# Kernel optimization log

Measured on AMD Instinct MI355X. Metric: run time of the kernel, lower is better.

Reference implementation:

```python
import jax, jax.numpy as jnp
import numpy as np

B, S, D = 1024, 256, 256  # batch, n_class, feature dim (g = n_component = 1)


def setup_inputs() -> dict:
    key = jax.random.key(0)
    k1, k2, k3 = jax.random.split(key, 3)
    x = jax.random.normal(k1, (B, D), dtype=jnp.float32)
    mu_p = jax.random.normal(k2, (S, 1, D), dtype=jnp.float32)
    sigma_p = jax.random.normal(k3, (S, 1, D, D), dtype=jnp.float32)
    return {"x": x, "mu_p": mu_p, "sigma_p": sigma_p}


def _log_probs(x, mu_p, sigma_p):
    sp = sigma_p[:, 0]            # (S, D, D), component index g=0
    mu = mu_p[:, 0]               # (S, D)
    # parameter_enforcing: m = sigma_p^T @ sigma_p (PSD);
    # mean of (real) eigenvalues of m == trace(m)/D, so the ridge term is
    # 0.01 * (trace(m)/D) * I, making sigma symmetric positive definite.
    m = jnp.einsum('skd,ske->sde', sp, sp)                      # (S, D, D)
    ridge = 0.01 * (jnp.trace(m, axis1=-2, axis2=-1) / D)       # (S,)
    sigma = m + ridge[:, None, None] * jnp.eye(D, dtype=m.dtype)
    # MVN log_prob via Cholesky: logdet = 2*sum(log diag L),
    # maha = || L^{-1} (x - mu) ||^2
    L = jnp.linalg.cholesky(sigma)                              # (S, D, D)
    logdet = 2.0 * jnp.sum(jnp.log(jnp.diagonal(L, axis1=-2, axis2=-1)), -1)  # (S,)
    diff = x[None, :, :] - mu[:, None, :]                       # (S, B, D)
    # batched triangular solve per class: y = L^{-1} diff^T -> (S, D, B)
    y = jax.vmap(lambda Ls, ds: jax.scipy.linalg.solve_triangular(Ls, ds.T, lower=True))(L, diff)
    maha = jnp.sum(y * y, axis=1)                               # (S, B)
    log2pi = jnp.log(2.0 * jnp.pi).astype(x.dtype)
    logp = -0.5 * (D * log2pi + logdet[:, None] + maha)         # (S, B)
    return logp.T                                               # (B, S)


def reference(x, mu_p, sigma_p):
    return _log_probs(x, mu_p, sigma_p)
```

## Files before the change

### kernel.cpp

```cpp
#include <hip/hip_runtime.h>
#include <math.h>


#define LOG2PI_D 470.4965290007924f

typedef __attribute__((ext_vector_type(8))) short bf16x8;
typedef __attribute__((ext_vector_type(4))) float f32x4;

__device__ __forceinline__ unsigned bf16rtn(float f) {
  unsigned u = __float_as_uint(f);
  return (u + 0x7FFFu + ((u >> 16) & 1u)) >> 16;
}
__device__ __forceinline__ unsigned packhl(float v) {
  unsigned h = bf16rtn(v);
  float hf = __uint_as_float(h << 16);
  unsigned l = bf16rtn(v - hf);
  return (h << 16) | l;
}

__global__ __launch_bounds__(256) void k_gram(const float* __restrict__ sp,
                                              float* __restrict__ L,
                                              float* __restrict__ ridge_out) {
  __shared__ unsigned Hb[4 * 128 * 20];
  unsigned* AH = Hb;
  unsigned* AL = Hb + 128 * 20;
  unsigned* BH = Hb + 2 * 128 * 20;
  unsigned* BL = Hb + 3 * 128 * 20;
  int p = blockIdx.y, s = blockIdx.x;
  int bi = (p ? 128 : 0), bj = (p == 2 ? 128 : 0);
  const float* A = sp + (size_t)s * 65536;
  float* C = L + (size_t)s * 65536;
  int tid = threadIdx.x, w = tid >> 6, lane = tid & 63;
  int q = lane >> 4, n = lane & 15;
  int mt_[2] = {w, 7 - w};
  f32x4 acc[2][8] = {};
  int c = tid & 127, g = tid >> 7;

  float va[16], vb[16];
#pragma unroll
  for (int u = 0; u < 16; ++u) {
    va[u] = A[(size_t)(g * 16 + u) * 256 + bi + c];
    if (p == 1) vb[u] = A[(size_t)(g * 16 + u) * 256 + bj + c];
  }

  for (int ks = 0; ks < 8; ++ks) {
    __syncthreads();
    {
      unsigned hw[8], lw[8];
#pragma unroll
      for (int m = 0; m < 8; ++m) {
        float v0 = va[2 * m], v1 = va[2 * m + 1];
        unsigned h0 = bf16rtn(v0), h1 = bf16rtn(v1);
        float r0 = v0 - __uint_as_float(h0 << 16);
        float r1 = v1 - __uint_as_float(h1 << 16);
        hw[m] = h0 | (h1 << 16);
        lw[m] = bf16rtn(r0) | (bf16rtn(r1) << 16);
      }
      *(uint4*)&AH[c * 20 + g * 8] = make_uint4(hw[0], hw[1], hw[2], hw[3]);
      *(uint4*)&AH[c * 20 + g * 8 + 4] = make_uint4(hw[4], hw[5], hw[6], hw[7]);
      *(uint4*)&AL[c * 20 + g * 8] = make_uint4(lw[0], lw[1], lw[2], lw[3]);
      *(uint4*)&AL[c * 20 + g * 8 + 4] = make_uint4(lw[4], lw[5], lw[6], lw[7]);
      if (p == 1) {
#pragma unroll
        for (int m = 0; m < 8; ++m) {
          float v0 = vb[2 * m], v1 = vb[2 * m + 1];
          unsigned h0 = bf16rtn(v0), h1 = bf16rtn(v1);
          float r0 = v0 - __uint_as_float(h0 << 16);
          float r1 = v1 - __uint_as_float(h1 << 16);
          hw[m] = h0 | (h1 << 16);
          lw[m] = bf16rtn(r0) | (bf16rtn(r1) << 16);
        }
        *(uint4*)&BH[c * 20 + g * 8] = make_uint4(hw[0], hw[1], hw[2], hw[3]);
        *(uint4*)&BH[c * 20 + g * 8 + 4] = make_uint4(hw[4], hw[5], hw[6], hw[7]);
        *(uint4*)&BL[c * 20 + g * 8] = make_uint4(lw[0], lw[1], lw[2], lw[3]);
        *(uint4*)&BL[c * 20 + g * 8 + 4] = make_uint4(lw[4], lw[5], lw[6], lw[7]);
      }
    }
    __syncthreads();
    if (ks < 7) {
      int r0g = (ks + 1) * 32 + g * 16;
#pragma unroll
      for (int u = 0; u < 16; ++u) {
        va[u] = A[(size_t)(r0g + u) * 256 + bi + c];
        if (p == 1) vb[u] = A[(size_t)(r0g + u) * 256 + bj + c];
      }
    }
    const unsigned* TBH = (p == 1) ? BH : AH;
    const unsigned* TBL = (p == 1) ? BL : AL;
    bf16x8 Ah[2], Al[2];
#pragma unroll
    for (int t = 0; t < 2; ++t) {
      int col = mt_[t] * 16 + n;
      Ah[t] = *(const bf16x8*)&AH[col * 20 + q * 4];
      Al[t] = *(const bf16x8*)&AL[col * 20 + q * 4];
    }
    int ntmax = (p == 1) ? 8 : (8 - w);
    for (int nt = 0; nt < ntmax; ++nt) {
      bf16x8 bh = *(const bf16x8*)&TBH[(nt * 16 + n) * 20 + q * 4];
      bf16x8 bl = *(const bf16x8*)&TBL[(nt * 16 + n) * 20 + q * 4];
#pragma unroll
      for (int t = 0; t < 2; ++t) {
        if (p == 1 || nt <= mt_[t]) {
          acc[t][nt] = __builtin_amdgcn_mfma_f32_16x16x32_bf16(Ah[t], bh, acc[t][nt], 0, 0, 0);
          acc[t][nt] = __builtin_amdgcn_mfma_f32_16x16x32_bf16(Ah[t], bl, acc[t][nt], 0, 0, 0);
          acc[t][nt] = __builtin_amdgcn_mfma_f32_16x16x32_bf16(Al[t], bh, acc[t][nt], 0, 0, 0);
        }
      }
    }
  }
  if (p != 1) {
    float dsum = 0.f;
#pragma unroll
    for (int t = 0; t < 2; ++t) {
      if ((n >> 2) == q) dsum += acc[t][mt_[t]][n & 3];
    }
    dsum += __shfl_down(dsum, 32, 64);
    dsum += __shfl_down(dsum, 16, 64);
    dsum += __shfl_down(dsum, 8, 64);
    dsum += __shfl_down(dsum, 4, 64);
    dsum += __shfl_down(dsum, 2, 64);
    dsum += __shfl_down(dsum, 1, 64);
    if (lane == 0) atomicAdd(&ridge_out[s], dsum * (0.01f / 256.0f));
  }
  float* slab = (float*)Hb;
  for (int t = 0; t < 2; ++t) {
    __syncthreads();
#pragma unroll
    for (int nt = 0; nt < 8; ++nt)
#pragma unroll
      for (int r = 0; r < 4; ++r)
        slab[w * 2048 + (q * 4 + r) * 128 + nt * 16 + n] = acc[t][nt][r];
    __syncthreads();
#pragma unroll
    for (int it = 0; it < 8; ++it) {
      int idx = tid + it * 256;
      int row = idx >> 5, c4 = idx & 31;
      int wsrc = row >> 4, r16 = row & 15;
      int rt = t ? (7 - wsrc) : wsrc;
      if (p == 1 || (c4 >> 2) <= rt) {
        int d = bi + rt * 16 + r16;
        *(float4*)(C + (size_t)d * 256 + bj + c4 * 4) =
            *(float4*)&slab[wsrc * 2048 + r16 * 128 + c4 * 4];
      }
    }
  }
}

__global__ __launch_bounds__(256) void k_panel(float* __restrict__ L,
                                               const float* __restrict__ ridge_buf,
                                               int kb) {
  extern __shared__ float lds[];
  float* P = lds;
  float* W = lds + 64 * 68;
  float* WT = lds + 2 * 64 * 68;
  float* T = lds + 3 * 64 * 68;
  int s = blockIdx.x;
  float* M = L + (size_t)s * 65536;
  int tid = threadIdx.x;
  int k4 = tid & 15, rb = tid >> 4;
  int ty = tid >> 4, tx = tid & 15;
  int base = kb * 64;
  float ridge = ridge_buf[s];

  for (int r = rb; r < 64; r += 16)
    *(float4*)&P[r * 68 + k4 * 4] = *(const float4*)(M + (size_t)(base + r) * 256 + base + k4 * 4);
  __syncthreads();
  if (tid < 64) P[tid * 68 + tid] += ridge;
  __syncthreads();
  {
    int eo = tid & 63, ro = tid >> 6;
    for (int cb = 0; cb < 16; ++cb) {
      int c0 = cb * 4;
      float g00 = P[c0 * 68 + c0];
      float g10 = P[(c0 + 1) * 68 + c0], g11 = P[(c0 + 1) * 68 + c0 + 1];
      float g20 = P[(c0 + 2) * 68 + c0], g21 = P[(c0 + 2) * 68 + c0 + 1],
            g22 = P[(c0 + 2) * 68 + c0 + 2];
      float g30 = P[(c0 + 3) * 68 + c0], g31 = P[(c0 + 3) * 68 + c0 + 1],
            g32 = P[(c0 + 3) * 68 + c0 + 2], g33 = P[(c0 + 3) * 68 + c0 + 3];
      float l00 = sqrtf(g00), r0 = 1.f / l00;
      float l10 = g10 * r0, l20 = g20 * r0, l30 = g30 * r0;
      float l11 = sqrtf(g11 - l10 * l10), r1 = 1.f / l11;
      float l21 = (g21 - l20 * l10) * r1, l31 = (g31 - l30 * l10) * r1;
      float l22 = sqrtf(g22 - l20 * l20 - l21 * l21), r2 = 1.f / l22;
      float l32 = (g32 - l30 * l20 - l31 * l21) * r2;
      float l33 = sqrtf(g33 - l30 * l30 - l31 * l31 - l32 * l32), r3 = 1.f / l33;
      int e = c0 + 4 + eo;
      if (e < 64) {
        float p0 = P[e * 68 + c0], p1 = P[e * 68 + c0 + 1];
        float p2 = P[e * 68 + c0 + 2], p3 = P[e * 68 + c0 + 3];
        float le0 = p0 * r0;
        float le1 = (p1 - le0 * l10) * r1;
        float le2 = (p2 - le0 * l20 - le1 * l21) * r2;
        float le3 = (p3 - le0 * l30 - le1 * l31 - le2 * l32) * r3;
        for (int r = c0 + 4 + ro; r < 64; r += 4) {
          float q0 = P[r * 68 + c0], q1 = P[r * 68 + c0 + 1];
          float q2 = P[r * 68 + c0 + 2], q3 = P[r * 68 + c0 + 3];
          float lr0 = q0 * r0;
          float lr1 = (q1 - lr0 * l10) * r1;
          float lr2 = (q2 - lr0 * l20 - lr1 * l21) * r2;
          float lr3 = (q3 - lr0 * l30 - lr1 * l31 - lr2 * l32) * r3;
          P[r * 68 + e] -= lr0 * le0 + lr1 * le1 + lr2 * le2 + lr3 * le3;
        }
      }
      __syncthreads();
    }
  }
  {
    int cb = tid >> 4, lane16 = tid & 15;
    int c0 = cb * 4;
    float g00 = P[c0 * 68 + c0];
    float g10 = P[(c0 + 1) * 68 + c0], g11 = P[(c0 + 1) * 68 + c0 + 1];
    float g20 = P[(c0 + 2) * 68 + c0], g21 = P[(c0 + 2) * 68 + c0 + 1],
          g22 = P[(c0 + 2) * 68 + c0 + 2];
    float g30 = P[(c0 + 3) * 68 + c0], g31 = P[(c0 + 3) * 68 + c0 + 1],
          g32 = P[(c0 + 3) * 68 + c0 + 2], g33 = P[(c0 + 3) * 68 + c0 + 3];
    float l00 = sqrtf(g00), r0 = 1.f / l00;
    float l10 = g10 * r0, l20 = g20 * r0, l30 = g30 * r0;
    float l11 = sqrtf(g11 - l10 * l10), r1 = 1.f / l11;
    float l21 = (g21 - l20 * l10) * r1, l31 = (g31 - l30 * l10) * r1;
    float l22 = sqrtf(g22 - l20 * l20 - l21 * l21), r2 = 1.f / l22;
    float l32 = (g32 - l30 * l20 - l31 * l21) * r2;
    float l33 = sqrtf(g33 - l30 * l30 - l31 * l31 - l32 * l32), r3 = 1.f / l33;
    float vals[4][4];
    int rows[4], nr = 0;
    for (int r = c0 + lane16; r < 64; r += 16) {
      int i = r - c0;
      if (i == 0) { vals[nr][0] = l00; vals[nr][1] = 0; vals[nr][2] = 0; vals[nr][3] = 0; }
      else if (i == 1) { vals[nr][0] = l10; vals[nr][1] = l11; vals[nr][2] = 0; vals[nr][3] = 0; }
      else if (i == 2) { vals[nr][0] = l20; vals[nr][1] = l21; vals[nr][2] = l22; vals[nr][3] = 0; }
      else if (i == 3) { vals[nr][0] = l30; vals[nr][1] = l31; vals[nr][2] = l32; vals[nr][3] = l33; }
      else {
        float q0 = P[r * 68 + c0], q1 = P[r * 68 + c0 + 1];
        float q2 = P[r * 68 + c0 + 2], q3 = P[r * 68 + c0 + 3];
        float lr0 = q0 * r0;
        float lr1 = (q1 - lr0 * l10) * r1;
        float lr2 = (q2 - lr0 * l20 - lr1 * l21) * r2;
        float lr3 = (q3 - lr0 * l30 - lr1 * l31 - lr2 * l32) * r3;
        vals[nr][0] = lr0; vals[nr][1] = lr1; vals[nr][2] = lr2; vals[nr][3] = lr3;
      }
      rows[nr++] = r;
    }
    __syncthreads();
    for (int u = 0; u < nr; ++u) {
      int r = rows[u];
      P[r * 68 + c0] = vals[u][0];
      P[r * 68 + c0 + 1] = vals[u][1];
      P[r * 68 + c0 + 2] = vals[u][2];
      P[r * 68 + c0 + 3] = vals[u][3];
    }
  }
  __syncthreads();
  if (tid < 64) {
    int c = tid;
    int rl = (c < 32) ? 32 : 64;
    for (int r = 0; r < c; ++r) W[r * 68 + c] = 0.f;
    W[c * 68 + c] = 1.0f / P[c * 68 + c];
    for (int r = c + 1; r < rl; ++r) {
      float a = 0.f;
      for (int k = c; k < r; ++k) a += P[r * 68 + k] * W[k * 68 + c];
      W[r * 68 + c] = -a / P[r * 68 + r];
    }
  }
  __syncthreads();
  {
    int r0 = (tid >> 4) * 2, c0 = (tid & 15) * 2;
    float a00 = 0, a01 = 0, a10 = 0, a11 = 0;
    for (int k = 0; k < 32; ++k) {
      float b0 = P[(32 + r0) * 68 + k], b1 = P[(33 + r0) * 68 + k];
      float w0 = W[k * 68 + c0], w1 = W[k * 68 + c0 + 1];
      a00 += b0 * w0; a01 += b0 * w1; a10 += b1 * w0; a11 += b1 * w1;
    }
    T[r0 * 68 + c0] = a00; T[r0 * 68 + c0 + 1] = a01;
    T[(r0 + 1) * 68 + c0] = a10; T[(r0 + 1) * 68 + c0 + 1] = a11;
  }
  __syncthreads();
  {
    int r0 = (tid >> 4) * 2, c0 = (tid & 15) * 2;
    float a00 = 0, a01 = 0, a10 = 0, a11 = 0;
    for (int k = 0; k < 32; ++k) {
      float i0 = W[(32 + r0) * 68 + 32 + k], i1 = W[(33 + r0) * 68 + 32 + k];
      float t0 = T[k * 68 + c0], t1 = T[k * 68 + c0 + 1];
      a00 += i0 * t0; a01 += i0 * t1; a10 += i1 * t0; a11 += i1 * t1;
    }
    W[(32 + r0) * 68 + c0] = -a00; W[(32 + r0) * 68 + c0 + 1] = -a01;
    W[(33 + r0) * 68 + c0] = -a10; W[(33 + r0) * 68 + c0 + 1] = -a11;
  }
  __syncthreads();
  for (int c = rb; c < 64; c += 16) {
    float4 v = *(float4*)&W[c * 68 + k4 * 4];
    WT[(k4 * 4 + 0) * 68 + c] = v.x;
    WT[(k4 * 4 + 1) * 68 + c] = v.y;
    WT[(k4 * 4 + 2) * 68 + c] = v.z;
    WT[(k4 * 4 + 3) * 68 + c] = v.w;
  }
  __syncthreads();
  for (int r = rb; r < 64; r += 16)
    *(float4*)(M + (size_t)(base + r) * 256 + base + k4 * 4) = *(float4*)&W[r * 68 + k4 * 4];
  int nrt = 3 - kb;
  for (int rt = 0; rt < nrt; ++rt) {
    int g0 = base + 64 + rt * 64;
    __syncthreads();
    for (int r = rb; r < 64; r += 16) {
      float4 v = *(const float4*)(M + (size_t)(g0 + r) * 256 + base + k4 * 4);
      T[(k4 * 4 + 0) * 68 + r] = v.x;
      T[(k4 * 4 + 1) * 68 + r] = v.y;
      T[(k4 * 4 + 2) * 68 + r] = v.z;
      T[(k4 * 4 + 3) * 68 + r] = v.w;
    }
    __syncthreads();
    float acc[4][4] = {};
    for (int k = 0; k < 64; ++k) {
      float a[4], b[4];
      *(float4*)a = *(float4*)&T[k * 68 + ty * 4];
      *(float4*)b = *(float4*)&WT[k * 68 + tx * 4];
#pragma unroll
      for (int i = 0; i < 4; ++i)
#pragma unroll
        for (int j = 0; j < 4; ++j) acc[i][j] += a[i] * b[j];
    }
    __syncthreads();
#pragma unroll
    for (int i = 0; i < 4; ++i)
      *(float4*)(M + (size_t)(g0 + ty * 4 + i) * 256 + base + tx * 4) =
          make_float4(acc[i][0], acc[i][1], acc[i][2], acc[i][3]);
#pragma unroll
    for (int i = 0; i < 4; ++i)
#pragma unroll
      for (int j = 0; j < 4; ++j) T[(tx * 4 + j) * 68 + ty * 4 + i] = acc[i][j];
    __syncthreads();
    for (int r = rb; r < 64; r += 16)
      *(float4*)(M + (size_t)(base + r) * 256 + g0 + k4 * 4) = *(float4*)&T[r * 68 + k4 * 4];
  }
}

__global__ __launch_bounds__(256) void k_trail(float* __restrict__ L, int kb) {
  extern __shared__ float lds[];
  float* Pi = lds;
  float* Pj = lds + 64 * 68;
  int p = blockIdx.y, s = blockIdx.x;
  int ti = 0, tj = 0, cnt = 0;
  for (int a = kb + 1; a < 4; ++a)
    for (int b = kb + 1; b <= a; ++b) {
      if (cnt == p) { ti = a; tj = b; }
      ++cnt;
    }
  float* M = L + (size_t)s * 65536;
  int tid = threadIdx.x, k4 = tid & 15, rb = tid >> 4;
  int ty = tid >> 4, tx = tid & 15;
  int base = kb * 64;
  for (int k = rb; k < 64; k += 16) {
    *(float4*)&Pi[k * 68 + k4 * 4] = *(const float4*)(M + (size_t)(base + k) * 256 + ti * 64 + k4 * 4);
    *(float4*)&Pj[k * 68 + k4 * 4] = *(const float4*)(M + (size_t)(base + k) * 256 + tj * 64 + k4 * 4);
  }
  float acc[4][4];
#pragma unroll
  for (int i = 0; i < 4; ++i)
    *(float4*)&acc[i][0] = *(const float4*)(M + (size_t)(ti * 64 + ty * 4 + i) * 256 + tj * 64 + tx * 4);
  __syncthreads();
  for (int k = 0; k < 64; ++k) {
    float a[4], b[4];
    *(float4*)a = *(float4*)&Pi[k * 68 + ty * 4];
    *(float4*)b = *(float4*)&Pj[k * 68 + tx * 4];
#pragma unroll
    for (int i = 0; i < 4; ++i)
#pragma unroll
      for (int j = 0; j < 4; ++j) acc[i][j] -= a[i] * b[j];
  }
#pragma unroll
  for (int i = 0; i < 4; ++i)
    *(float4*)(M + (size_t)(ti * 64 + ty * 4 + i) * 256 + tj * 64 + tx * 4) =
        make_float4(acc[i][0], acc[i][1], acc[i][2], acc[i][3]);
}

__global__ __launch_bounds__(256) void k_invcol(float* __restrict__ Lw) {
  extern __shared__ float lds[];
  float* Bcol = lds;
  float* LW = lds + 3 * 64 * 68;
  float* Cs = LW + 64 * 68;
  int j = blockIdx.y, s = blockIdx.x;
  float* M = Lw + (size_t)s * 65536;
  unsigned* M32 = (unsigned*)M;
  int tid = threadIdx.x, k4 = tid & 15, rb = tid >> 4;
  int ty = tid >> 4, tx = tid & 15;

  for (int r = rb; r < 64; r += 16)
    *(float4*)&Bcol[r * 68 + k4 * 4] =
        *(const float4*)(M + (size_t)(j * 64 + r) * 256 + j * 64 + k4 * 4);
  __syncthreads();

  for (int i = j + 1; i < 4; ++i) {
    float acc[4][4] = {};
    for (int kk = j; kk < i; ++kk) {
      __syncthreads();
      for (int k = rb; k < 64; k += 16)
        *(float4*)&LW[k * 68 + k4 * 4] =
            *(const float4*)(M + (size_t)(kk * 64 + k) * 256 + i * 64 + k4 * 4);
      __syncthreads();
      float* Bk = Bcol + (kk - j) * 64 * 68;
#pragma unroll 4
      for (int k = 0; k < 64; ++k) {
        float a[4], b[4];
        *(float4*)a = *(float4*)&LW[k * 68 + ty * 4];
        *(float4*)b = *(float4*)&Bk[k * 68 + tx * 4];
#pragma unroll
        for (int r = 0; r < 4; ++r)
#pragma unroll
          for (int c = 0; c < 4; ++c) acc[r][c] += a[r] * b[c];
      }
    }
    __syncthreads();
#pragma unroll
    for (int r = 0; r < 4; ++r)
      *(float4*)&Cs[(ty * 4 + r) * 68 + tx * 4] =
          make_float4(acc[r][0], acc[r][1], acc[r][2], acc[r][3]);
    for (int r = rb; r < 64; r += 16) {
      float4 v = *(const float4*)(M + (size_t)(i * 64 + r) * 256 + i * 64 + k4 * 4);
      LW[(k4 * 4 + 0) * 68 + r] = v.x;
      LW[(k4 * 4 + 1) * 68 + r] = v.y;
      LW[(k4 * 4 + 2) * 68 + r] = v.z;
      LW[(k4 * 4 + 3) * 68 + r] = v.w;
    }
    __syncthreads();
    float d[4][4] = {};
#pragma unroll 4
    for (int k = 0; k < 64; ++k) {
      float a[4], b[4];
      *(float4*)a = *(float4*)&LW[k * 68 + ty * 4];
      *(float4*)b = *(float4*)&Cs[k * 68 + tx * 4];
#pragma unroll
      for (int r = 0; r < 4; ++r)
#pragma unroll
        for (int c = 0; c < 4; ++c) d[r][c] -= a[r] * b[c];
    }
    float* Bi = Bcol + (i - j) * 64 * 68;
#pragma unroll
    for (int r = 0; r < 4; ++r) {
      if (i < 3)
        *(float4*)&Bi[(ty * 4 + r) * 68 + tx * 4] =
            make_float4(d[r][0], d[r][1], d[r][2], d[r][3]);
      uint4 pu;
      pu.x = packhl(d[r][0]); pu.y = packhl(d[r][1]);
      pu.z = packhl(d[r][2]); pu.w = packhl(d[r][3]);
      *(uint4*)(M32 + (size_t)(i * 64 + ty * 4 + r) * 256 + j * 64 + tx * 4) = pu;
    }
    __syncthreads();
  }
}

__global__ __launch_bounds__(512) void k_maha(const float* __restrict__ x,
                                              const float* __restrict__ mu_p,
                                              const float* __restrict__ Lw,
                                              float* __restrict__ out) {
  __shared__ __align__(16) short Bh[128 * 40];
  __shared__ __align__(16) short Bl[128 * 40];
  __shared__ float Red[1025];
  int s = blockIdx.x, b0 = blockIdx.y * 128;
  const float* Mf = Lw + (size_t)s * 65536;
  const unsigned* M32 = (const unsigned*)Mf;
  int tid = threadIdx.x, w = tid >> 6, lane = tid & 63;
  int q = lane >> 4, n = lane & 15;
  int mt_[2] = {w, 15 - w};
  f32x4 acc[2][8] = {};

  for (int ks = 0; ks < 8; ++ks) {
    __syncthreads();
    {
      int b = tid >> 2, q8 = tid & 3;
      const float* xp = x + (size_t)(b0 + b) * 256 + ks * 32 + q8 * 8;
      const float* mp = mu_p + (size_t)s * 256 + ks * 32 + q8 * 8;
      float4 xa = ((const float4*)xp)[0], xb = ((const float4*)xp)[1];
      float4 ma = ((const float4*)mp)[0], mb = ((const float4*)mp)[1];
      float dv[8] = {xa.x - ma.x, xa.y - ma.y, xa.z - ma.z, xa.w - ma.w,
                     xb.x - mb.x, xb.y - mb.y, xb.z - mb.z, xb.w - mb.w};
      unsigned h[8], l[8];
#pragma unroll
      for (int jj = 0; jj < 8; ++jj) {
        h[jj] = bf16rtn(dv[jj]);
        float hf = __uint_as_float(h[jj] << 16);
        l[jj] = bf16rtn(dv[jj] - hf);
      }
      *(uint4*)&Bh[b * 40 + q8 * 8] =
          make_uint4(h[0] | (h[1] << 16), h[2] | (h[3] << 16),
                     h[4] | (h[5] << 16), h[6] | (h[7] << 16));
      *(uint4*)&Bl[b * 40 + q8 * 8] =
          make_uint4(l[0] | (l[1] << 16), l[2] | (l[3] << 16),
                     l[4] | (l[5] << 16), l[6] | (l[7] << 16));
    }
    __syncthreads();
    bf16x8 Ah[2], Al[2];
    bool act[2];
#pragma unroll
    for (int t = 0; t < 2; ++t) {
      int mt = mt_[t];
      act[t] = ks < ((mt + 2) >> 1);
      if (act[t]) {
        const unsigned* ap = M32 + (size_t)(mt * 16 + n) * 256 + ks * 32 + q * 8;
        uint4 u0 = *(const uint4*)ap;
        uint4 u1 = *(const uint4*)(ap + 4);
        unsigned uu[8] = {u0.x, u0.y, u0.z, u0.w, u1.x, u1.y, u1.z, u1.w};
        if ((ks >> 1) == (mt >> 2)) {
#pragma unroll
          for (int jj = 0; jj < 8; ++jj) {
            float f = __uint_as_float(uu[jj]);
            unsigned hh = bf16rtn(f);
            float hf = __uint_as_float(hh << 16);
            Ah[t][jj] = (short)hh;
            Al[t][jj] = (short)bf16rtn(f - hf);
          }
        } else {
#pragma unroll
          for (int jj = 0; jj < 8; ++jj) {
            Ah[t][jj] = (short)(uu[jj] >> 16);
            Al[t][jj] = (short)(uu[jj] & 0xffffu);
          }
        }
      }
    }
#pragma unroll
    for (int bsub = 0; bsub < 8; ++bsub) {
      bf16x8 bh = *(const bf16x8*)&Bh[(bsub * 16 + n) * 40 + q * 8];
      bf16x8 bl = *(const bf16x8*)&Bl[(bsub * 16 + n) * 40 + q * 8];
#pragma unroll
      for (int t = 0; t < 2; ++t) {
        if (act[t]) {
          acc[t][bsub] = __builtin_amdgcn_mfma_f32_16x16x32_bf16(Ah[t], bh, acc[t][bsub], 0, 0, 0);
          acc[t][bsub] = __builtin_amdgcn_mfma_f32_16x16x32_bf16(Ah[t], bl, acc[t][bsub], 0, 0, 0);
          acc[t][bsub] = __builtin_amdgcn_mfma_f32_16x16x32_bf16(Al[t], bh, acc[t][bsub], 0, 0, 0);
        }
      }
    }
  }
#pragma unroll
  for (int bsub = 0; bsub < 8; ++bsub) {
    float v = 0.f;
#pragma unroll
    for (int t = 0; t < 2; ++t)
#pragma unroll
      for (int r = 0; r < 4; ++r) v += acc[t][bsub][r] * acc[t][bsub][r];
    v += __shfl_xor(v, 16, 64);
    v += __shfl_xor(v, 32, 64);
    if (lane < 16) Red[w * 128 + bsub * 16 + lane] = v;
  }
  if (w == 0) {
    float ld = 0.f;
#pragma unroll
    for (int c = 0; c < 4; ++c)
      ld += logf(Mf[(size_t)(c * 64 + lane) * 256 + c * 64 + lane]);
    ld += __shfl_down(ld, 32, 64);
    ld += __shfl_down(ld, 16, 64);
    ld += __shfl_down(ld, 8, 64);
    ld += __shfl_down(ld, 4, 64);
    ld += __shfl_down(ld, 2, 64);
    ld += __shfl_down(ld, 1, 64);
    if (lane == 0) Red[1024] = ld;
  }
  __syncthreads();
  if (tid < 128) {
    float mh = 0.f;
#pragma unroll
    for (int w2 = 0; w2 < 8; ++w2) mh += Red[w2 * 128 + tid];
    out[(size_t)(b0 + tid) * 256 + s] = -0.5f * (LOG2PI_D - 2.0f * Red[1024] + mh);
  }
}

extern "C" void kernel_launch(void* const* d_in, const int* in_sizes, int n_in,
                              void* d_out, int out_size, void* d_ws, size_t ws_size,
                              hipStream_t stream) {
  const float* x = (const float*)d_in[0];
  const float* mu = (const float*)d_in[1];
  const float* sp = (const float*)d_in[2];
  float* out = (float*)d_out;
  float* L = (float*)d_ws;

  const int panel_lds = 4 * 64 * 68 * 4;
  const int trail_lds = 2 * 64 * 68 * 4;
  const int invc_lds = 5 * 64 * 68 * 4;
  (void)hipFuncSetAttribute((const void*)k_panel,
                            hipFuncAttributeMaxDynamicSharedMemorySize, panel_lds);
  (void)hipFuncSetAttribute((const void*)k_trail,
                            hipFuncAttributeMaxDynamicSharedMemorySize, trail_lds);
  (void)hipFuncSetAttribute((const void*)k_invcol,
                            hipFuncAttributeMaxDynamicSharedMemorySize, invc_lds);

  k_gram<<<dim3(256, 3), 256, 0, stream>>>(sp, L, out);
  const int npairs[4] = {6, 3, 1, 0};
  for (int kb = 0; kb < 4; ++kb) {
    k_panel<<<256, 256, panel_lds, stream>>>(L, out, kb);
    if (npairs[kb])
      k_trail<<<dim3(256, npairs[kb]), 256, trail_lds, stream>>>(L, kb);
  }
  k_invcol<<<dim3(256, 3), 256, invc_lds, stream>>>(L);
  k_maha<<<dim3(256, 8), 512, 0, stream>>>(x, mu, L, out);
}
```

Baseline: 623.5 us.

## Fuse panel, trailing-update and inverse kernels into one per-class factor kernel

Replaces the sequence of per-block panel, trailing-update and inverse-column launches with a single kernel that loops over all four block steps and then computes the inverse blocks for one class per workgroup. This removes about eight kernel launches and the gaps between them. The trade-off is less parallelism: the trailing updates and the inverse column work used to spread over several workgroups per class, and now one 256-thread block per class does them serially, using 256 blocks in total with larger LDS per block.

Result: slower. 654.7 us (+5.0%).

```diff
diff --git a/kernel.cpp b/kernel.cpp
--- a/kernel.cpp
+++ b/kernel.cpp
@@ -146,9 +146,8 @@
   }
 }
 
-__global__ __launch_bounds__(256) void k_panel(float* __restrict__ L,
-                                               const float* __restrict__ ridge_buf,
-                                               int kb) {
+__global__ __launch_bounds__(256) void k_factor(float* __restrict__ L,
+                                                const float* __restrict__ ridge_buf) {
   extern __shared__ float lds[];
   float* P = lds;
   float* W = lds + 64 * 68;
@@ -156,20 +155,60 @@
   float* T = lds + 3 * 64 * 68;
   int s = blockIdx.x;
   float* M = L + (size_t)s * 65536;
+  unsigned* M32 = (unsigned*)M;
   int tid = threadIdx.x;
   int k4 = tid & 15, rb = tid >> 4;
   int ty = tid >> 4, tx = tid & 15;
-  int base = kb * 64;
   float ridge = ridge_buf[s];
 
-  for (int r = rb; r < 64; r += 16)
-    *(float4*)&P[r * 68 + k4 * 4] = *(const float4*)(M + (size_t)(base + r) * 256 + base + k4 * 4);
-  __syncthreads();
-  if (tid < 64) P[tid * 68 + tid] += ridge;
-  __syncthreads();
-  {
-    int eo = tid & 63, ro = tid >> 6;
-    for (int cb = 0; cb < 16; ++cb) {
+  for (int kb = 0; kb < 4; ++kb) {
+    int base = kb * 64;
+    __syncthreads();
+    for (int r = rb; r < 64; r += 16)
+      *(float4*)&P[r * 68 + k4 * 4] = *(const float4*)(M + (size_t)(base + r) * 256 + base + k4 * 4);
+    __syncthreads();
+    if (tid < 64) P[tid * 68 + tid] += ridge;
+    __syncthreads();
+    {
+      int eo = tid & 63, ro = tid >> 6;
+      for (int cb = 0; cb < 16; ++cb) {
+        int c0 = cb * 4;
+        float g00 = P[c0 * 68 + c0];
+        float g10 = P[(c0 + 1) * 68 + c0], g11 = P[(c0 + 1) * 68 + c0 + 1];
+        float g20 = P[(c0 + 2) * 68 + c0], g21 = P[(c0 + 2) * 68 + c0 + 1],
+              g22 = P[(c0 + 2) * 68 + c0 + 2];
+        float g30 = P[(c0 + 3) * 68 + c0], g31 = P[(c0 + 3) * 68 + c0 + 1],
+              g32 = P[(c0 + 3) * 68 + c0 + 2], g33 = P[(c0 + 3) * 68 + c0 + 3];
+        float l00 = sqrtf(g00), r0 = 1.f / l00;
+        float l10 = g10 * r0, l20 = g20 * r0, l30 = g30 * r0;
+        float l11 = sqrtf(g11 - l10 * l10), r1 = 1.f / l11;
+        float l21 = (g21 - l20 * l10) * r1, l31 = (g31 - l30 * l10) * r1;
+        float l22 = sqrtf(g22 - l20 * l20 - l21 * l21), r2 = 1.f / l22;
+        float l32 = (g32 - l30 * l20 - l31 * l21) * r2;
+        float l33 = sqrtf(g33 - l30 * l30 - l31 * l31 - l32 * l32), r3 = 1.f / l33;
+        int e = c0 + 4 + eo;
+        if (e < 64) {
+          float p0 = P[e * 68 + c0], p1 = P[e * 68 + c0 + 1];
+          float p2 = P[e * 68 + c0 + 2], p3 = P[e * 68 + c0 + 3];
+          float le0 = p0 * r0;
+          float le1 = (p1 - le0 * l10) * r1;
+          float le2 = (p2 - le0 * l20 - le1 * l21) * r2;
+          float le3 = (p3 - le0 * l30 - le1 * l31 - le2 * l32) * r3;
+          for (int r = c0 + 4 + ro; r < 64; r += 4) {
+            float q0 = P[r * 68 + c0], q1 = P[r * 68 + c0 + 1];
+            float q2 = P[r * 68 + c0 + 2], q3 = P[r * 68 + c0 + 3];
+            float lr0 = q0 * r0;
+            float lr1 = (q1 - lr0 * l10) * r1;
+            float lr2 = (q2 - lr0 * l20 - lr1 * l21) * r2;
+            float lr3 = (q3 - lr0 * l30 - lr1 * l31 - lr2 * l32) * r3;
+            P[r * 68 + e] -= lr0 * le0 + lr1 * le1 + lr2 * le2 + lr3 * le3;
+          }
+        }
+        __syncthreads();
+      }
+    }
+    {
+      int cb = tid >> 4, lane16 = tid & 15;
       int c0 = cb * 4;
       float g00 = P[c0 * 68 + c0];
       float g10 = P[(c0 + 1) * 68 + c0], g11 = P[(c0 + 1) * 68 + c0 + 1];
@@ -184,266 +223,217 @@
       float l22 = sqrtf(g22 - l20 * l20 - l21 * l21), r2 = 1.f / l22;
       float l32 = (g32 - l30 * l20 - l31 * l21) * r2;
       float l33 = sqrtf(g33 - l30 * l30 - l31 * l31 - l32 * l32), r3 = 1.f / l33;
-      int e = c0 + 4 + eo;
-      if (e < 64) {
-        float p0 = P[e * 68 + c0], p1 = P[e * 68 + c0 + 1];
-        float p2 = P[e * 68 + c0 + 2], p3 = P[e * 68 + c0 + 3];
-        float le0 = p0 * r0;
-        float le1 = (p1 - le0 * l10) * r1;
-        float le2 = (p2 - le0 * l20 - le1 * l21) * r2;
-        float le3 = (p3 - le0 * l30 - le1 * l31 - le2 * l32) * r3;
-        for (int r = c0 + 4 + ro; r < 64; r += 4) {
+      float vals[4][4];
+      int rows[4], nr = 0;
+      for (int r = c0 + lane16; r < 64; r += 16) {
+        int i = r - c0;
+        if (i == 0) { vals[nr][0] = l00; vals[nr][1] = 0; vals[nr][2] = 0; vals[nr][3] = 0; }
+        else if (i == 1) { vals[nr][0] = l10; vals[nr][1] = l11; vals[nr][2] = 0; vals[nr][3] = 0; }
+        else if (i == 2) { vals[nr][0] = l20; vals[nr][1] = l21; vals[nr][2] = l22; vals[nr][3] = 0; }
+        else if (i == 3) { vals[nr][0] = l30; vals[nr][1] = l31; vals[nr][2] = l32; vals[nr][3] = l33; }
+        else {
           float q0 = P[r * 68 + c0], q1 = P[r * 68 + c0 + 1];
           float q2 = P[r * 68 + c0 + 2], q3 = P[r * 68 + c0 + 3];
           float lr0 = q0 * r0;
           float lr1 = (q1 - lr0 * l10) * r1;
           float lr2 = (q2 - lr0 * l20 - lr1 * l21) * r2;
           float lr3 = (q3 - lr0 * l30 - lr1 * l31 - lr2 * l32) * r3;
-          P[r * 68 + e] -= lr0 * le0 + lr1 * le1 + lr2 * le2 + lr3 * le3;
-        }
-      }
-      __syncthreads();
-    }
-  }
-  {
-    int cb = tid >> 4, lane16 = tid & 15;
-    int c0 = cb * 4;
-    float g00 = P[c0 * 68 + c0];
-    float g10 = P[(c0 + 1) * 68 + c0], g11 = P[(c0 + 1) * 68 + c0 + 1];
-    float g20 = P[(c0 + 2) * 68 + c0], g21 = P[(c0 + 2) * 68 + c0 + 1],
-          g22 = P[(c0 + 2) * 68 + c0 + 2];
-    float g30 = P[(c0 + 3) * 68 + c0], g31 = P[(c0 + 3) * 68 + c0 + 1],
-          g32 = P[(c0 + 3) * 68 + c0 + 2], g33 = P[(c0 + 3) * 68 + c0 + 3];
-    float l00 = sqrtf(g00), r0 = 1.f / l00;
-    float l10 = g10 * r0, l20 = g20 * r0, l30 = g30 * r0;
-    float l11 = sqrtf(g11 - l10 * l10), r1 = 1.f / l11;
-    float l21 = (g21 - l20 * l10) * r1, l31 = (g31 - l30 * l10) * r1;
-    float l22 = sqrtf(g22 - l20 * l20 - l21 * l21), r2 = 1.f / l22;
-    float l32 = (g32 - l30 * l20 - l31 * l21) * r2;
-    float l33 = sqrtf(g33 - l30 * l30 - l31 * l31 - l32 * l32), r3 = 1.f / l33;
-    float vals[4][4];
-    int rows[4], nr = 0;
-    for (int r = c0 + lane16; r < 64; r += 16) {
-      int i = r - c0;
-      if (i == 0) { vals[nr][0] = l00; vals[nr][1] = 0; vals[nr][2] = 0; vals[nr][3] = 0; }
-      else if (i == 1) { vals[nr][0] = l10; vals[nr][1] = l11; vals[nr][2] = 0; vals[nr][3] = 0; }
-      else if (i == 2) { vals[nr][0] = l20; vals[nr][1] = l21; vals[nr][2] = l22; vals[nr][3] = 0; }
-      else if (i == 3) { vals[nr][0] = l30; vals[nr][1] = l31; vals[nr][2] = l32; vals[nr][3] = l33; }
-      else {
-        float q0 = P[r * 68 + c0], q1 = P[r * 68 + c0 + 1];
-        float q2 = P[r * 68 + c0 + 2], q3 = P[r * 68 + c0 + 3];
-        float lr0 = q0 * r0;
-        float lr1 = (q1 - lr0 * l10) * r1;
-        float lr2 = (q2 - lr0 * l20 - lr1 * l21) * r2;
-        float lr3 = (q3 - lr0 * l30 - lr1 * l31 - lr2 * l32) * r3;
-        vals[nr][0] = lr0; vals[nr][1] = lr1; vals[nr][2] = lr2; vals[nr][3] = lr3;
-      }
-      rows[nr++] = r;
-    }
-    __syncthreads();
-    for (int u = 0; u < nr; ++u) {
-      int r = rows[u];
-      P[r * 68 + c0] = vals[u][0];
-      P[r * 68 + c0 + 1] = vals[u][1];
-      P[r * 68 + c0 + 2] = vals[u][2];
-      P[r * 68 + c0 + 3] = vals[u][3];
-    }
-  }
-  __syncthreads();
-  if (tid < 64) {
-    int c = tid;
-    int rl = (c < 32) ? 32 : 64;
-    for (int r = 0; r < c; ++r) W[r * 68 + c] = 0.f;
-    W[c * 68 + c] = 1.0f / P[c * 68 + c];
-    for (int r = c + 1; r < rl; ++r) {
-      float a = 0.f;
-      for (int k = c; k < r; ++k) a += P[r * 68 + k] * W[k * 68 + c];
-      W[r * 68 + c] = -a / P[r * 68 + r];
-    }
-  }
-  __syncthreads();
-  {
-    int r0 = (tid >> 4) * 2, c0 = (tid & 15) * 2;
-    float a00 = 0, a01 = 0, a10 = 0, a11 = 0;
-    for (int k = 0; k < 32; ++k) {
-      float b0 = P[(32 + r0) * 68 + k], b1 = P[(33 + r0) * 68 + k];
-      float w0 = W[k * 68 + c0], w1 = W[k * 68 + c0 + 1];
-      a00 += b0 * w0; a01 += b0 * w1; a10 += b1 * w0; a11 += b1 * w1;
-    }
-    T[r0 * 68 + c0] = a00; T[r0 * 68 + c0 + 1] = a01;
-    T[(r0 + 1) * 68 + c0] = a10; T[(r0 + 1) * 68 + c0 + 1] = a11;
-  }
-  __syncthreads();
-  {
-    int r0 = (tid >> 4) * 2, c0 = (tid & 15) * 2;
-    float a00 = 0, a01 = 0, a10 = 0, a11 = 0;
-    for (int k = 0; k < 32; ++k) {
-      float i0 = W[(32 + r0) * 68 + 32 + k], i1 = W[(33 + r0) * 68 + 32 + k];
-      float t0 = T[k * 68 + c0], t1 = T[k * 68 + c0 + 1];
-      a00 += i0 * t0; a01 += i0 * t1; a10 += i1 * t0; a11 += i1 * t1;
-    }
-    W[(32 + r0) * 68 + c0] = -a00; W[(32 + r0) * 68 + c0 + 1] = -a01;
-    W[(33 + r0) * 68 + c0] = -a10; W[(33 + r0) * 68 + c0 + 1] = -a11;
-  }
-  __syncthreads();
-  for (int c = rb; c < 64; c += 16) {
-    float4 v = *(float4*)&W[c * 68 + k4 * 4];
-    WT[(k4 * 4 + 0) * 68 + c] = v.x;
-    WT[(k4 * 4 + 1) * 68 + c] = v.y;
-    WT[(k4 * 4 + 2) * 68 + c] = v.z;
-    WT[(k4 * 4 + 3) * 68 + c] = v.w;
-  }
-  __syncthreads();
-  for (int r = rb; r < 64; r += 16)
-    *(float4*)(M + (size_t)(base + r) * 256 + base + k4 * 4) = *(float4*)&W[r * 68 + k4 * 4];
-  int nrt = 3 - kb;
-  for (int rt = 0; rt < nrt; ++rt) {
-    int g0 = base + 64 + rt * 64;
-    __syncthreads();
-    for (int r = rb; r < 64; r += 16) {
-      float4 v = *(const float4*)(M + (size_t)(g0 + r) * 256 + base + k4 * 4);
-      T[(k4 * 4 + 0) * 68 + r] = v.x;
-      T[(k4 * 4 + 1) * 68 + r] = v.y;
-      T[(k4 * 4 + 2) * 68 + r] = v.z;
-      T[(k4 * 4 + 3) * 68 + r] = v.w;
-    }
-    __syncthreads();
-    float acc[4][4] = {};
-    for (int k = 0; k < 64; ++k) {
-      float a[4], b[4];
-      *(float4*)a = *(float4*)&T[k * 68 + ty * 4];
-      *(float4*)b = *(float4*)&WT[k * 68 + tx * 4];
-#pragma unroll
-      for (int i = 0; i < 4; ++i)
-#pragma unroll
-        for (int j = 0; j < 4; ++j) acc[i][j] += a[i] * b[j];
-    }
-    __syncthreads();
-#pragma unroll
-    for (int i = 0; i < 4; ++i)
-      *(float4*)(M + (size_t)(g0 + ty * 4 + i) * 256 + base + tx * 4) =
-          make_float4(acc[i][0], acc[i][1], acc[i][2], acc[i][3]);
-#pragma unroll
-    for (int i = 0; i < 4; ++i)
-#pragma unroll
-      for (int j = 0; j < 4; ++j) T[(tx * 4 + j) * 68 + ty * 4 + i] = acc[i][j];
+          vals[nr][0] = lr0; vals[nr][1] = lr1; vals[nr][2] = lr2; vals[nr][3] = lr3;
+        }
+        rows[nr++] = r;
+      }
+      __syncthreads();
+      for (int u = 0; u < nr; ++u) {
+        int r = rows[u];
+        P[r * 68 + c0] = vals[u][0];
+        P[r * 68 + c0 + 1] = vals[u][1];
+        P[r * 68 + c0 + 2] = vals[u][2];
+        P[r * 68 + c0 + 3] = vals[u][3];
+      }
+    }
+    __syncthreads();
+    if (tid < 64) {
+      int c = tid;
+      int rl = (c < 32) ? 32 : 64;
+      for (int r = 0; r < c; ++r) W[r * 68 + c] = 0.f;
+      W[c * 68 + c] = 1.0f / P[c * 68 + c];
+      for (int r = c + 1; r < rl; ++r) {
+        float a = 0.f;
+        for (int k = c; k < r; ++k) a += P[r * 68 + k] * W[k * 68 + c];
+        W[r * 68 + c] = -a / P[r * 68 + r];
+      }
+    }
+    __syncthreads();
+    {
+      int r0 = (tid >> 4) * 2, c0 = (tid & 15) * 2;
+      float a00 = 0, a01 = 0, a10 = 0, a11 = 0;
+      for (int k = 0; k < 32; ++k) {
+        float b0 = P[(32 + r0) * 68 + k], b1 = P[(33 + r0) * 68 + k];
+        float w0 = W[k * 68 + c0], w1 = W[k * 68 + c0 + 1];
+        a00 += b0 * w0; a01 += b0 * w1; a10 += b1 * w0; a11 += b1 * w1;
+      }
+      T[r0 * 68 + c0] = a00; T[r0 * 68 + c0 + 1] = a01;
+      T[(r0 + 1) * 68 + c0] = a10; T[(r0 + 1) * 68 + c0 + 1] = a11;
+    }
+    __syncthreads();
+    {
+      int r0 = (tid >> 4) * 2, c0 = (tid & 15) * 2;
+      float a00 = 0, a01 = 0, a10 = 0, a11 = 0;
+      for (int k = 0; k < 32; ++k) {
+        float i0 = W[(32 + r0) * 68 + 32 + k], i1 = W[(33 + r0) * 68 + 32 + k];
+        float t0 = T[k * 68 + c0], t1 = T[k * 68 + c0 + 1];
+        a00 += i0 * t0; a01 += i0 * t1; a10 += i1 * t0; a11 += i1 * t1;
+      }
+      W[(32 + r0) * 68 + c0] = -a00; W[(32 + r0) * 68 + c0 + 1] = -a01;
+      W[(33 + r0) * 68 + c0] = -a10; W[(33 + r0) * 68 + c0 + 1] = -a11;
+    }
+    __syncthreads();
+    for (int c = rb; c < 64; c += 16) {
+      float4 v = *(float4*)&W[c * 68 + k4 * 4];
+      WT[(k4 * 4 + 0) * 68 + c] = v.x;
+      WT[(k4 * 4 + 1) * 68 + c] = v.y;
+      WT[(k4 * 4 + 2) * 68 + c] = v.z;
+      WT[(k4 * 4 + 3) * 68 + c] = v.w;
+    }
     __syncthreads();
     for (int r = rb; r < 64; r += 16)
-      *(float4*)(M + (size_t)(base + r) * 256 + g0 + k4 * 4) = *(float4*)&T[r * 68 + k4 * 4];
-  }
-}
-
-__global__ __launch_bounds__(256) void k_trail(float* __restrict__ L, int kb) {
-  extern __shared__ float lds[];
-  float* Pi = lds;
-  float* Pj = lds + 64 * 68;
-  int p = blockIdx.y, s = blockIdx.x;
-  int ti = 0, tj = 0, cnt = 0;
-  for (int a = kb + 1; a < 4; ++a)
-    for (int b = kb + 1; b <= a; ++b) {
-      if (cnt == p) { ti = a; tj = b; }
-      ++cnt;
-    }
-  float* M = L + (size_t)s * 65536;
-  int tid = threadIdx.x, k4 = tid & 15, rb = tid >> 4;
-  int ty = tid >> 4, tx = tid & 15;
-  int base = kb * 64;
-  for (int k = rb; k < 64; k += 16) {
-    *(float4*)&Pi[k * 68 + k4 * 4] = *(const float4*)(M + (size_t)(base + k) * 256 + ti * 64 + k4 * 4);
-    *(float4*)&Pj[k * 68 + k4 * 4] = *(const float4*)(M + (size_t)(base + k) * 256 + tj * 64 + k4 * 4);
-  }
-  float acc[4][4];
-#pragma unroll
-  for (int i = 0; i < 4; ++i)
-    *(float4*)&acc[i][0] = *(const float4*)(M + (size_t)(ti * 64 + ty * 4 + i) * 256 + tj * 64 + tx * 4);
-  __syncthreads();
-  for (int k = 0; k < 64; ++k) {
-    float a[4], b[4];
-    *(float4*)a = *(float4*)&Pi[k * 68 + ty * 4];
-    *(float4*)b = *(float4*)&Pj[k * 68 + tx * 4];
-#pragma unroll
-    for (int i = 0; i < 4; ++i)
-#pragma unroll
-      for (int j = 0; j < 4; ++j) acc[i][j] -= a[i] * b[j];
-  }
-#pragma unroll
-  for (int i = 0; i < 4; ++i)
-    *(float4*)(M + (size_t)(ti * 64 + ty * 4 + i) * 256 + tj * 64 + tx * 4) =
-        make_float4(acc[i][0], acc[i][1], acc[i][2], acc[i][3]);
-}
-
-__global__ __launch_bounds__(256) void k_invcol(float* __restrict__ Lw) {
-  extern __shared__ float lds[];
-  float* Bcol = lds;
-  float* LW = lds + 3 * 64 * 68;
-  float* Cs = LW + 64 * 68;
-  int j = blockIdx.y, s = blockIdx.x;
-  float* M = Lw + (size_t)s * 65536;
-  unsigned* M32 = (unsigned*)M;
-  int tid = threadIdx.x, k4 = tid & 15, rb = tid >> 4;
-  int ty = tid >> 4, tx = tid & 15;
-
-  for (int r = rb; r < 64; r += 16)
-    *(float4*)&Bcol[r * 68 + k4 * 4] =
-        *(const float4*)(M + (size_t)(j * 64 + r) * 256 + j * 64 + k4 * 4);
-  __syncthreads();
-
-  for (int i = j + 1; i < 4; ++i) {
-    float acc[4][4] = {};
-    for (int kk = j; kk < i; ++kk) {
-      __syncthreads();
-      for (int k = rb; k < 64; k += 16)
-        *(float4*)&LW[k * 68 + k4 * 4] =
-            *(const float4*)(M + (size_t)(kk * 64 + k) * 256 + i * 64 + k4 * 4);
-      __syncthreads();
-      float* Bk = Bcol + (kk - j) * 64 * 68;
-#pragma unroll 4
+      *(float4*)(M + (size_t)(base + r) * 256 + base + k4 * 4) = *(float4*)&W[r * 68 + k4 * 4];
+    int nrt = 3 - kb;
+    for (int rt = 0; rt < nrt; ++rt) {
+      int g0 = base + 64 + rt * 64;
+      __syncthreads();
+      for (int r = rb; r < 64; r += 16) {
+        float4 v = *(const float4*)(M + (size_t)(g0 + r) * 256 + base + k4 * 4);
+        T[(k4 * 4 + 0) * 68 + r] = v.x;
+        T[(k4 * 4 + 1) * 68 + r] = v.y;
+        T[(k4 * 4 + 2) * 68 + r] = v.z;
+        T[(k4 * 4 + 3) * 68 + r] = v.w;
+      }
+      __syncthreads();
+      float acc[4][4] = {};
       for (int k = 0; k < 64; ++k) {
         float a[4], b[4];
-        *(float4*)a = *(float4*)&LW[k * 68 + ty * 4];
-        *(float4*)b = *(float4*)&Bk[k * 68 + tx * 4];
+        *(float4*)a = *(float4*)&T[k * 68 + ty * 4];
+        *(float4*)b = *(float4*)&WT[k * 68 + tx * 4];
+#pragma unroll
+        for (int i = 0; i < 4; ++i)
+#pragma unroll
+          for (int j = 0; j < 4; ++j) acc[i][j] += a[i] * b[j];
+      }
+      __syncthreads();
+#pragma unroll
+      for (int i = 0; i < 4; ++i)
+        *(float4*)(M + (size_t)(g0 + ty * 4 + i) * 256 + base + tx * 4) =
+            make_float4(acc[i][0], acc[i][1], acc[i][2], acc[i][3]);
+#pragma unroll
+      for (int i = 0; i < 4; ++i)
+#pragma unroll
+        for (int j = 0; j < 4; ++j) T[(tx * 4 + j) * 68 + ty * 4 + i] = acc[i][j];
+      __syncthreads();
+      for (int r = rb; r < 64; r += 16)
+        *(float4*)(M + (size_t)(base + r) * 256 + g0 + k4 * 4) = *(float4*)&T[r * 68 + k4 * 4];
+    }
+    for (int ti = kb + 1; ti < 4; ++ti) {
+      for (int tj = kb + 1; tj <= ti; ++tj) {
+        __syncthreads();
+        for (int k = rb; k < 64; k += 16) {
+          *(float4*)&P[k * 68 + k4 * 4] =
+              *(const float4*)(M + (size_t)(base + k) * 256 + ti * 64 + k4 * 4);
+          *(float4*)&W[k * 68 + k4 * 4] =
+              *(const float4*)(M + (size_t)(base + k) * 256 + tj * 64 + k4 * 4);
+        }
+        float acc[4][4];
+#pragma unroll
+        for (int i = 0; i < 4; ++i)
+          *(float4*)&acc[i][0] =
+              *(const float4*)(M + (size_t)(ti * 64 + ty * 4 + i) * 256 + tj * 64 + tx * 4);
+        __syncthreads();
+        for (int k = 0; k < 64; ++k) {
+          float a[4], b[4];
+          *(float4*)a = *(float4*)&P[k * 68 + ty * 4];
+          *(float4*)b = *(float4*)&W[k * 68 + tx * 4];
+#pragma unroll
+          for (int i = 0; i < 4; ++i)
+#pragma unroll
+            for (int j = 0; j < 4; ++j) acc[i][j] -= a[i] * b[j];
+        }
+#pragma unroll
+        for (int i = 0; i < 4; ++i)
+          *(float4*)(M + (size_t)(ti * 64 + ty * 4 + i) * 256 + tj * 64 + tx * 4) =
+              make_float4(acc[i][0], acc[i][1], acc[i][2], acc[i][3]);
+      }
+    }
+  }
+
+  {
+    float* Bcol = lds;
+    float* LW = lds + 3 * 64 * 68;
+    float* Cs = LW + 64 * 68;
+    for (int j = 0; j < 3; ++j) {
+      __syncthreads();
+      for (int r = rb; r < 64; r += 16)
+        *(float4*)&Bcol[r * 68 + k4 * 4] =
+            *(const float4*)(M + (size_t)(j * 64 + r) * 256 + j * 64 + k4 * 4);
+      __syncthreads();
+
+      for (int i = j + 1; i < 4; ++i) {
+        float acc[4][4] = {};
+        for (int kk = j; kk < i; ++kk) {
+          __syncthreads();
+          for (int k = rb; k < 64; k += 16)
+            *(float4*)&LW[k * 68 + k4 * 4] =
+                *(const float4*)(M + (size_t)(kk * 64 + k) * 256 + i * 64 + k4 * 4);
+          __syncthreads();
+          float* Bk = Bcol + (kk - j) * 64 * 68;
+#pragma unroll 4
+          for (int k = 0; k < 64; ++k) {
+            float a[4], b[4];
+            *(float4*)a = *(float4*)&LW[k * 68 + ty * 4];
+            *(float4*)b = *(float4*)&Bk[k * 68 + tx * 4];
+#pragma unroll
+            for (int r = 0; r < 4; ++r)
+#pragma unroll
+              for (int cc = 0; cc < 4; ++cc) acc[r][cc] += a[r] * b[cc];
+          }
+        }
+        __syncthreads();
 #pragma unroll
         for (int r = 0; r < 4; ++r)
-#pragma unroll
-          for (int c = 0; c < 4; ++c) acc[r][c] += a[r] * b[c];
-      }
-    }
-    __syncthreads();
-#pragma unroll
-    for (int r = 0; r < 4; ++r)
-      *(float4*)&Cs[(ty * 4 + r) * 68 + tx * 4] =
-          make_float4(acc[r][0], acc[r][1], acc[r][2], acc[r][3]);
-    for (int r = rb; r < 64; r += 16) {
-      float4 v = *(const float4*)(M + (size_t)(i * 64 + r) * 256 + i * 64 + k4 * 4);
-      LW[(k4 * 4 + 0) * 68 + r] = v.x;
-      LW[(k4 * 4 + 1) * 68 + r] = v.y;
-      LW[(k4 * 4 + 2) * 68 + r] = v.z;
-      LW[(k4 * 4 + 3) * 68 + r] = v.w;
-    }
-    __syncthreads();
-    float d[4][4] = {};
+          *(float4*)&Cs[(ty * 4 + r) * 68 + tx * 4] =
+              make_float4(acc[r][0], acc[r][1], acc[r][2], acc[r][3]);
+        for (int r = rb; r < 64; r += 16) {
+          float4 v = *(const float4*)(M + (size_t)(i * 64 + r) * 256 + i * 64 + k4 * 4);
+          LW[(k4 * 4 + 0) * 68 + r] = v.x;
+          LW[(k4 * 4 + 1) * 68 + r] = v.y;
+          LW[(k4 * 4 + 2) * 68 + r] = v.z;
+          LW[(k4 * 4 + 3) * 68 + r] = v.w;
+        }
+        __syncthreads();
+        float d[4][4] = {};
 #pragma unroll 4
-    for (int k = 0; k < 64; ++k) {
-      float a[4], b[4];
-      *(float4*)a = *(float4*)&LW[k * 68 + ty * 4];
-      *(float4*)b = *(float4*)&Cs[k * 68 + tx * 4];
-#pragma unroll
-      for (int r = 0; r < 4; ++r)
-#pragma unroll
-        for (int c = 0; c < 4; ++c) d[r][c] -= a[r] * b[c];
-    }
-    float* Bi = Bcol + (i - j) * 64 * 68;
-#pragma unroll
-    for (int r = 0; r < 4; ++r) {
-      if (i < 3)
-        *(float4*)&Bi[(ty * 4 + r) * 68 + tx * 4] =
-            make_float4(d[r][0], d[r][1], d[r][2], d[r][3]);
-      uint4 pu;
-      pu.x = packhl(d[r][0]); pu.y = packhl(d[r][1]);
-      pu.z = packhl(d[r][2]); pu.w = packhl(d[r][3]);
-      *(uint4*)(M32 + (size_t)(i * 64 + ty * 4 + r) * 256 + j * 64 + tx * 4) = pu;
-    }
-    __syncthreads();
+        for (int k = 0; k < 64; ++k) {
+          float a[4], b[4];
+          *(float4*)a = *(float4*)&LW[k * 68 + ty * 4];
+          *(float4*)b = *(float4*)&Cs[k * 68 + tx * 4];
+#pragma unroll
+          for (int r = 0; r < 4; ++r)
+#pragma unroll
+            for (int cc = 0; cc < 4; ++cc) d[r][cc] -= a[r] * b[cc];
+        }
+        float* Bi = Bcol + (i - j) * 64 * 68;
+#pragma unroll
+        for (int r = 0; r < 4; ++r) {
+          if (i < 3)
+            *(float4*)&Bi[(ty * 4 + r) * 68 + tx * 4] =
+                make_float4(d[r][0], d[r][1], d[r][2], d[r][3]);
+          uint4 pu;
+          pu.x = packhl(d[r][0]); pu.y = packhl(d[r][1]);
+          pu.z = packhl(d[r][2]); pu.w = packhl(d[r][3]);
+          *(uint4*)(M32 + (size_t)(i * 64 + ty * 4 + r) * 256 + j * 64 + tx * 4) = pu;
+        }
+        __syncthreads();
+      }
+    }
   }
 }
 
@@ -572,23 +562,11 @@
   float* out = (float*)d_out;
   float* L = (float*)d_ws;
 
-  const int panel_lds = 4 * 64 * 68 * 4;
-  const int trail_lds = 2 * 64 * 68 * 4;
-  const int invc_lds = 5 * 64 * 68 * 4;
-  (void)hipFuncSetAttribute((const void*)k_panel,
-                            hipFuncAttributeMaxDynamicSharedMemorySize, panel_lds);
-  (void)hipFuncSetAttribute((const void*)k_trail,
-                            hipFuncAttributeMaxDynamicSharedMemorySize, trail_lds);
-  (void)hipFuncSetAttribute((const void*)k_invcol,
-                            hipFuncAttributeMaxDynamicSharedMemorySize, invc_lds);
+  const int fact_lds = 5 * 64 * 68 * 4;
+  (void)hipFuncSetAttribute((const void*)k_factor,
+                            hipFuncAttributeMaxDynamicSharedMemorySize, fact_lds);
 
   k_gram<<<dim3(256, 3), 256, 0, stream>>>(sp, L, out);
-  const int npairs[4] = {6, 3, 1, 0};
-  for (int kb = 0; kb < 4; ++kb) {
-    k_panel<<<256, 256, panel_lds, stream>>>(L, out, kb);
-    if (npairs[kb])
-      k_trail<<<dim3(256, npairs[kb]), 256, trail_lds, stream>>>(L, kb);
-  }
-  k_invcol<<<dim3(256, 3), 256, invc_lds, stream>>>(L);
+  k_factor<<<256, 256, fact_lds, stream>>>(L, out);
   k_maha<<<dim3(256, 8), 512, 0, stream>>>(x, mu, L, out);
 }
```
